# Kernel tuning notes

Hardware: AMD Instinct MI355X
Metric: run time of the kernel (lower is better)

Reference implementation:

```python
import jax, jax.numpy as jnp
import numpy as np


def rotary_pos_emb(x):
    # x: [b, h, l, k]; interleaved rotary embedding (pairs are (0,1),(2,3),...)
    dim = x.shape[-1]
    seq = x.shape[-2]
    ts = jnp.arange(0, dim, 2, dtype=jnp.float32)
    inv_freqs = 10000.0 ** (-ts / dim)                      # [dim/2]
    grid = jnp.arange(seq, dtype=jnp.float32)[:, None] * inv_freqs[None, :]  # [l, dim/2]
    sin_embs = jnp.repeat(jnp.sin(grid), 2, axis=-1)[None]  # [1, l, dim] (interleaved repeat)
    cos_embs = jnp.repeat(jnp.cos(grid), 2, axis=-1)[None]
    x1, x2 = x[..., ::2], x[..., 1::2]
    xs = jnp.stack([-x2, x1], axis=-1).reshape(x.shape)     # interleave (-x2, x1)
    return x * cos_embs + xs * sin_embs


def setup_inputs() -> dict:
    key = jax.random.key(0)
    ks = jax.random.split(key, 5)
    b, l, d = 2, 2048, 1024
    scale = 1.0 / np.sqrt(d)
    return {
        "x": jax.random.normal(ks[0], (b, l, d), dtype=jnp.float32),
        "Wq": jax.random.normal(ks[1], (d, d), dtype=jnp.float32) * scale,
        "Wk": jax.random.normal(ks[2], (d, d), dtype=jnp.float32) * scale,
        "Wv": jax.random.normal(ks[3], (d, d), dtype=jnp.float32) * scale,
        "Wo": jax.random.normal(ks[4], (d, d), dtype=jnp.float32) * scale,
        "is_training": 0,
    }


def reference(x, Wq, Wk, Wv, Wo, is_training):
    n_heads = 16
    b, l, d = x.shape
    k_size = d // n_heads
    # NOTE: module scales q by 1/sqrt(model_size), not 1/sqrt(key_size)
    q = (x @ Wq) / jnp.sqrt(jnp.float32(d))
    q = q.reshape(b, l, n_heads, k_size).transpose(0, 2, 1, 3)  # b h l k
    k = (x @ Wk).reshape(b, l, n_heads, k_size).transpose(0, 2, 1, 3)
    v = (x @ Wv).reshape(b, l, n_heads, k_size).transpose(0, 2, 1, 3)
    q = rotary_pos_emb(q)
    k = rotary_pos_emb(k)
    logits = jnp.einsum('bhik,bhjk->bhij', q, k)  # no mask, no dropout (eval)
    a = jax.nn.softmax(logits, axis=-1)
    y = jnp.einsum('bhij,bhjv->bhiv', a, v)
    y = y.transpose(0, 2, 1, 3).reshape(b, l, d)  # b l (h v)
    return y @ Wo
```

## Files before the change

kernel.cpp:

```cpp
#include <hip/hip_runtime.h>
#include <stdint.h>

typedef unsigned short u16;
typedef unsigned int u32;
using short8 = __attribute__((ext_vector_type(8))) short;
using f32x4  = __attribute__((ext_vector_type(4))) float;
using f32x16 = __attribute__((ext_vector_type(16))) float;

typedef __attribute__((address_space(1))) unsigned int gu32;
typedef __attribute__((address_space(3))) unsigned int lu32;

__device__ __forceinline__ void gl2lds16(const u16* g, u16* lds_wave_base) {
    __builtin_amdgcn_global_load_lds(
        (gu32*)(uintptr_t)(const void*)g,
        (lu32*)(uint32_t)(uintptr_t)(void*)lds_wave_base,
        16, 0, 0);
}

__device__ inline float bf2f(u16 u) {
    union { unsigned int i; float f; } v;
    v.i = ((unsigned int)u) << 16;
    return v.f;
}
__device__ inline u16 f2bf(float f) {
    union { float f; unsigned int i; } v;
    v.f = f;
    unsigned int x = v.i;
    return (u16)((x + 0x7fffu + ((x >> 16) & 1u)) >> 16);
}
__device__ inline u32 f2bf_trunc_u32(float f) {
    union { float f; unsigned int i; } v;
    v.f = f;
    return v.i >> 16;
}

__global__ __launch_bounds__(256) void prep(
    const float* __restrict__ x, u16* __restrict__ xb,
    const float* __restrict__ w0, const float* __restrict__ w1,
    const float* __restrict__ w2, const float* __restrict__ w3,
    u16* __restrict__ t0, u16* __restrict__ t1,
    u16* __restrict__ t2, u16* __restrict__ t3,
    float2* __restrict__ tab)
{
    int tx = threadIdx.x, ty = threadIdx.y;
    int tid = ty * 32 + tx;
    int z = blockIdx.z;
    if (z == 4) {
        int bidx = blockIdx.y * 32 + blockIdx.x;
        if (bidx < 256) {
            int idx = bidx * 256 + tid;
            int pos = idx >> 5, pi = idx & 31;
            const float l2_10000_over_32 = 0.41524101186f;
            float ang = (float)pos *
                __builtin_amdgcn_exp2f(-(float)pi * l2_10000_over_32);
            float sn, cs;
            __sincosf(ang, &sn, &cs);
            tab[idx] = make_float2(cs, sn);
        }
        return;
    }
    if (z >= 5) {
        int i = (((z - 5) * 1024 + blockIdx.y * 32 + blockIdx.x) * 256 + tid) * 4;
        float4 v = *(const float4*)(x + i);
        ushort4 o;
        o.x = f2bf(v.x); o.y = f2bf(v.y); o.z = f2bf(v.z); o.w = f2bf(v.w);
        *(ushort4*)(xb + i) = o;
        return;
    }
    __shared__ u16 tile[32][33];
    const float* src; u16* dst;
    switch (z) {
        case 0:  src = w0; dst = t0; break;
        case 1:  src = w1; dst = t1; break;
        case 2:  src = w2; dst = t2; break;
        default: src = w3; dst = t3; break;
    }
    int c0 = blockIdx.x * 32, r0 = blockIdx.y * 32;
    #pragma unroll
    for (int i = 0; i < 4; i++)
        tile[ty + i * 8][tx] = f2bf(src[(size_t)(r0 + ty + i * 8) * 1024 + c0 + tx]);
    __syncthreads();
    #pragma unroll
    for (int i = 0; i < 4; i++)
        dst[(size_t)(c0 + ty + i * 8) * 1024 + r0 + tx] = tile[tx][ty + i * 8];
}

__global__ __launch_bounds__(256) void gemm_qkv(
    const u16* __restrict__ A, const u16* __restrict__ Bt,
    const float2* __restrict__ ropetab,
    u16* __restrict__ Qb, u16* __restrict__ Kb, u16* __restrict__ VT)
{
    __shared__ __align__(16) char smem[128 * 136 * 2];
    u16* As = (u16*)smem;
    u16* Bs = (u16*)(smem + 16384);

    const int tid  = threadIdx.x;
    const int lane = tid & 63;
    const int wid  = tid >> 6;
    const int quad = lane >> 4;
    const int l15  = lane & 15;
    const int wm   = wid >> 1, wn = wid & 1;

    const int m0 = blockIdx.y * 128;
    const int n0 = blockIdx.x * 128;
    const int mat = n0 >> 10;
    const int ln0 = n0 & 1023;

    f32x4 acc[4][4] = {};

    for (int k0 = 0; k0 < 1024; k0 += 64) {
        #pragma unroll
        for (int it = 0; it < 4; it++) {
            int c   = it * 256 + tid;
            int row = c >> 3;
            int col = ((c & 7) ^ (row & 7)) * 8;
            u16* lbA = &As[(size_t)(it * 256 + wid * 64) * 8];
            u16* lbB = &Bs[(size_t)(it * 256 + wid * 64) * 8];
            gl2lds16(&A [(size_t)(m0 + row) * 1024 + k0 + col], lbA);
            gl2lds16(&Bt[(size_t)(n0 + row) * 1024 + k0 + col], lbB);
        }
        __syncthreads();

        #pragma unroll
        for (int s = 0; s < 2; s++) {
            short8 a[4], b[4];
            #pragma unroll
            for (int i = 0; i < 4; i++) {
                int ra = wm * 64 + i * 16 + l15;
                int rb = wn * 64 + i * 16 + l15;
                a[i] = *(const short8*)(&As[ra * 64 + (((s * 4 + quad) ^ (ra & 7)) * 8)]);
                b[i] = *(const short8*)(&Bs[rb * 64 + (((s * 4 + quad) ^ (rb & 7)) * 8)]);
            }
            #pragma unroll
            for (int i = 0; i < 4; i++)
                #pragma unroll
                for (int j = 0; j < 4; j++)
                    acc[i][j] = __builtin_amdgcn_mfma_f32_16x16x32_bf16(a[i], b[j], acc[i][j], 0, 0, 0);
        }
        __syncthreads();
    }

    if (mat < 2) {
        u16* C = (mat == 0) ? Qb : Kb;
        const float scale = (mat == 0) ? (0.03125f * 1.44269504f) : 1.0f;
        const int odd = l15 & 1;
        #pragma unroll
        for (int i = 0; i < 4; i++)
            #pragma unroll
            for (int j = 0; j < 4; j++)
                #pragma unroll
                for (int r = 0; r < 4; r++) {
                    int lrow = wm * 64 + i * 16 + quad * 4 + r;
                    int col  = ln0 + wn * 64 + j * 16 + l15;
                    int pos  = (m0 + lrow) & 2047;
                    float v  = acc[i][j][r] * scale;
                    float vp = __shfl_xor(v, 1);
                    float2 sc = ropetab[pos * 32 + ((col & 63) >> 1)];
                    float outv = odd ? (v * sc.x + vp * sc.y)
                                     : (v * sc.x - vp * sc.y);
                    C[(size_t)(m0 + lrow) * 1024 + col] = f2bf(outv);
                }
    } else {
        u16* T = (u16*)smem;
        __syncthreads();
        #pragma unroll
        for (int i = 0; i < 4; i++)
            #pragma unroll
            for (int j = 0; j < 4; j++)
                #pragma unroll
                for (int r = 0; r < 4; r++) {
                    int lrow = wm * 64 + i * 16 + quad * 4 + r;
                    int lcol = wn * 64 + j * 16 + l15;
                    T[lcol * 136 + lrow] = f2bf(acc[i][j][r]);
                }
        __syncthreads();
        int bb2 = m0 >> 11, pos0 = m0 & 2047;
        #pragma unroll
        for (int itc = 0; itc < 8; itc++) {
            int c  = itc * 256 + tid;
            int ch = c >> 4;
            int px = (c & 15) * 8;
            int head = (ln0 + ch) >> 6;
            size_t dst = ((size_t)(bb2 * 16 + head) * 64 + (ch & 63)) * 2048
                         + pos0 + px;
            *(uint4*)(&VT[dst]) = *(const uint4*)(&T[ch * 136 + px]);
        }
    }
}

__global__ __launch_bounds__(256) void gemm_out(
    const u16* __restrict__ A, const u16* __restrict__ Bt, float* __restrict__ C)
{
    __shared__ __align__(16) u16 As[128 * 64];
    __shared__ __align__(16) u16 Bs[128 * 64];

    const int tid  = threadIdx.x;
    const int lane = tid & 63;
    const int wid  = tid >> 6;
    const int quad = lane >> 4;
    const int l15  = lane & 15;
    const int wm   = wid >> 1, wn = wid & 1;

    const int m0 = blockIdx.y * 128;
    const int n0 = blockIdx.x * 128;

    f32x4 acc[4][4] = {};

    for (int k0 = 0; k0 < 1024; k0 += 64) {
        #pragma unroll
        for (int it = 0; it < 4; it++) {
            int c   = it * 256 + tid;
            int row = c >> 3;
            int col = ((c & 7) ^ (row & 7)) * 8;
            u16* lbA = &As[(size_t)(it * 256 + wid * 64) * 8];
            u16* lbB = &Bs[(size_t)(it * 256 + wid * 64) * 8];
            gl2lds16(&A [(size_t)(m0 + row) * 1024 + k0 + col], lbA);
            gl2lds16(&Bt[(size_t)(n0 + row) * 1024 + k0 + col], lbB);
        }
        __syncthreads();

        #pragma unroll
        for (int s = 0; s < 2; s++) {
            short8 a[4], b[4];
            #pragma unroll
            for (int i = 0; i < 4; i++) {
                int ra = wm * 64 + i * 16 + l15;
                int rb = wn * 64 + i * 16 + l15;
                a[i] = *(const short8*)(&As[ra * 64 + (((s * 4 + quad) ^ (ra & 7)) * 8)]);
                b[i] = *(const short8*)(&Bs[rb * 64 + (((s * 4 + quad) ^ (rb & 7)) * 8)]);
            }
            #pragma unroll
            for (int i = 0; i < 4; i++)
                #pragma unroll
                for (int j = 0; j < 4; j++)
                    acc[i][j] = __builtin_amdgcn_mfma_f32_16x16x32_bf16(a[i], b[j], acc[i][j], 0, 0, 0);
        }
        __syncthreads();
    }

    #pragma unroll
    for (int i = 0; i < 4; i++)
        #pragma unroll
        for (int j = 0; j < 4; j++)
            #pragma unroll
            for (int r = 0; r < 4; r++) {
                int row = m0 + wm * 64 + i * 16 + quad * 4 + r;
                int col = n0 + wn * 64 + j * 16 + l15;
                C[(size_t)row * 1024 + col] = acc[i][j][r];
            }
}

__global__ __launch_bounds__(256) void attn(
    const u16* __restrict__ Q, const u16* __restrict__ Kb,
    const u16* __restrict__ VT, u16* __restrict__ Y)
{
    __shared__ __align__(16) u16 Ks [128 * 64];
    __shared__ __align__(16) u16 VTs[64 * 128];
    __shared__ __align__(16) u16 Ps [4][32 * 72];

    const int tid  = threadIdx.x;
    const int lane = tid & 63, wid = tid >> 6;
    const int l31  = lane & 31, hi = lane >> 5;

    const int bh = blockIdx.x;
    const int qt = blockIdx.y;
    const int bb = bh >> 4, h = bh & 15;

    const size_t base = ((size_t)bb * 2048) * 1024 + (size_t)h * 64;

    short8 qf[4];
    {
        const u16* qp = Q + base
                      + ((size_t)qt * 128 + wid * 32 + l31) * 1024 + hi * 8;
        #pragma unroll
        for (int s = 0; s < 4; s++)
            qf[s] = *(const short8*)(qp + s * 16);
    }

    f32x16 o0 = {}, o1 = {};
    float lsum = 0.0f;

    for (int j0 = 0; j0 < 2048; j0 += 128) {
        __syncthreads();
        #pragma unroll
        for (int it = 0; it < 4; it++) {
            int c = it * 256 + tid;
            int rk = c >> 3, ck = ((c & 7)  ^ (rk & 7))  * 8;
            int rv = c >> 4, cv = ((c & 15) ^ (rv & 15)) * 8;
            u16* lbK = &Ks [(size_t)(it * 256 + wid * 64) * 8];
            u16* lbV = &VTs[(size_t)(it * 256 + wid * 64) * 8];
            gl2lds16(&Kb[base + (size_t)(j0 + rk) * 1024 + ck], lbK);
            gl2lds16(&VT[((size_t)bh * 64 + rv) * 2048 + j0 + cv], lbV);
        }
        __syncthreads();

        f32x16 st[4];
        #pragma unroll
        for (int t = 0; t < 4; t++) {
            int key = t * 32 + l31;
            f32x16 z = {};
            __builtin_amdgcn_s_setprio(1);
            #pragma unroll
            for (int s = 0; s < 4; s++) {
                int chunk = ((2 * s + hi) ^ (key & 7)) * 8;
                short8 kf = *(const short8*)(&Ks[key * 64 + chunk]);
                z = __builtin_amdgcn_mfma_f32_32x32x16_bf16(kf, qf[s], z, 0, 0, 0);
            }
            __builtin_amdgcn_s_setprio(0);
            st[t] = z;
        }

        u16* ps = Ps[wid];
        #pragma unroll
        for (int hh = 0; hh < 2; hh++) {
            #pragma unroll
            for (int tt = 0; tt < 2; tt++) {
                int t = hh * 2 + tt;
                #pragma unroll
                for (int g = 0; g < 4; g++) {
                    float p0 = __builtin_amdgcn_exp2f(st[t][4 * g + 0]);
                    float p1 = __builtin_amdgcn_exp2f(st[t][4 * g + 1]);
                    float p2 = __builtin_amdgcn_exp2f(st[t][4 * g + 2]);
                    float p3 = __builtin_amdgcn_exp2f(st[t][4 * g + 3]);
                    lsum += (p0 + p1) + (p2 + p3);
                    uint2 w;
                    w.x = f2bf_trunc_u32(p0) | (f2bf_trunc_u32(p1) << 16);
                    w.y = f2bf_trunc_u32(p2) | (f2bf_trunc_u32(p3) << 16);
                    int lk = tt * 32 + g * 8 + hi * 4;
                    *(uint2*)(&ps[l31 * 72 + lk]) = w;
                }
            }
            asm volatile("s_waitcnt lgkmcnt(0)" ::: "memory");

            #pragma unroll
            for (int s = 0; s < 4; s++) {
                int koff = s * 16 + hi * 8;
                short8 pf = *(const short8*)(&ps[l31 * 72 + koff]);
                int kch = hh * 8 + 2 * s + hi;
                short8 v0 = *(const short8*)(&VTs[l31 * 128 + ((kch ^ (l31 & 15)) * 8)]);
                short8 v1 = *(const short8*)(&VTs[(32 + l31) * 128 + ((kch ^ ((32 + l31) & 15)) * 8)]);
                __builtin_amdgcn_s_setprio(1);
                o0 = __builtin_amdgcn_mfma_f32_32x32x16_bf16(pf, v0, o0, 0, 0, 0);
                o1 = __builtin_amdgcn_mfma_f32_32x32x16_bf16(pf, v1, o1, 0, 0, 0);
                __builtin_amdgcn_s_setprio(0);
            }
            asm volatile("" ::: "memory");
        }
    }

    lsum += __shfl_xor(lsum, 32);
    float linv = 1.0f / lsum;

    size_t qrow0 = (size_t)qt * 128 + wid * 32;
    #pragma unroll
    for (int half = 0; half < 2; half++) {
        f32x16 o = half ? o1 : o0;
        #pragma unroll
        for (int reg = 0; reg < 16; reg++) {
            int qrow = (reg & 3) + 8 * (reg >> 2) + 4 * hi;
            float nv = o[reg] * __shfl(linv, qrow);
            Y[base + (qrow0 + qrow) * 1024 + half * 32 + l31] = f2bf(nv);
        }
    }
}

extern "C" void kernel_launch(void* const* d_in, const int* in_sizes, int n_in,
                              void* d_out, int out_size, void* d_ws, size_t ws_size,
                              hipStream_t stream)
{
    const float* x  = (const float*)d_in[0];
    const float* Wq = (const float*)d_in[1];
    const float* Wk = (const float*)d_in[2];
    const float* Wv = (const float*)d_in[3];
    const float* Wo = (const float*)d_in[4];
    float* out = (float*)d_out;

    char* ws = (char*)d_ws;
    u16*    xb    = (u16*)   (ws + (0ull  << 20));
    u16*    WqkvT = (u16*)   (ws + (8ull  << 20));
    u16*    WoT   = (u16*)   (ws + (14ull << 20));
    u16*    Qb    = (u16*)   (ws + (16ull << 20));
    u16*    Kb    = (u16*)   (ws + (24ull << 20));
    u16*    VTb   = (u16*)   (ws + (32ull << 20));
    u16*    Yb    = (u16*)   (ws + (40ull << 20));
    float2* tab   = (float2*)(ws + (48ull << 20));

    prep<<<dim3(32, 32, 9), dim3(32, 8), 0, stream>>>(
        x, xb, Wq, Wk, Wv, Wo,
        WqkvT, WqkvT + (1024ull * 1024), WqkvT + (2048ull * 1024), WoT, tab);
    gemm_qkv<<<dim3(24, 32), 256, 0, stream>>>(xb, WqkvT, tab, Qb, Kb, VTb);
    attn<<<dim3(32, 16), 256, 0, stream>>>(Qb, Kb, VTb, Yb);
    gemm_out<<<dim3(8, 32), 256, 0, stream>>>(Yb, WoT, out);
}
```

Baseline: 201.3 us.

## Prefetch next K/V tile into registers to overlap loads with attention compute

Replaces the direct global-to-LDS loads of each K and V^T tile with register staging. The next tile's global loads are issued into registers before the compute of the current tile, then written to LDS at the start of the next iteration. This is meant to hide global memory latency behind the QK^T/softmax/PV MFMA work. It adds eight uint4 registers per thread and sets a two-blocks-per-CU launch bound, which may constrain register allocation.

```diff
diff --git a/kernel.cpp b/kernel.cpp
--- a/kernel.cpp
+++ b/kernel.cpp
@@ -250,7 +250,7 @@
             }
 }
 
-__global__ __launch_bounds__(256) void attn(
+__global__ __launch_bounds__(256, 2) void attn(
     const u16* __restrict__ Q, const u16* __restrict__ Kb,
     const u16* __restrict__ VT, u16* __restrict__ Y)
 {
@@ -277,21 +277,54 @@
             qf[s] = *(const short8*)(qp + s * 16);
     }
 
+    const int c0 = tid,        c1 = 256 + tid,
+              c2 = 512 + tid,  c3 = 768 + tid;
+    const int rk0 = c0 >> 3, ck0 = ((c0 & 7) ^ (rk0 & 7)) * 8;
+    const int rk1 = c1 >> 3, ck1 = ((c1 & 7) ^ (rk1 & 7)) * 8;
+    const int rk2 = c2 >> 3, ck2 = ((c2 & 7) ^ (rk2 & 7)) * 8;
+    const int rk3 = c3 >> 3, ck3 = ((c3 & 7) ^ (rk3 & 7)) * 8;
+    const int rv0 = c0 >> 4, cv0 = ((c0 & 15) ^ (rv0 & 15)) * 8;
+    const int rv1 = c1 >> 4, cv1 = ((c1 & 15) ^ (rv1 & 15)) * 8;
+    const int rv2 = c2 >> 4, cv2 = ((c2 & 15) ^ (rv2 & 15)) * 8;
+    const int rv3 = c3 >> 4, cv3 = ((c3 & 15) ^ (rv3 & 15)) * 8;
+    const u16* pK = Kb + base;
+    const u16* pV = VT + ((size_t)bh * 64) * 2048;
+    const size_t oK0 = (size_t)rk0 * 1024 + ck0, oK1 = (size_t)rk1 * 1024 + ck1;
+    const size_t oK2 = (size_t)rk2 * 1024 + ck2, oK3 = (size_t)rk3 * 1024 + ck3;
+    const size_t oV0 = (size_t)rv0 * 2048 + cv0, oV1 = (size_t)rv1 * 2048 + cv1;
+    const size_t oV2 = (size_t)rv2 * 2048 + cv2, oV3 = (size_t)rv3 * 2048 + cv3;
+
+    uint4 k0r, k1r, k2r, k3r, v0r, v1r, v2r, v3r;
+#define LOADREGS(J0)                                                        \
+    do {                                                                    \
+        const size_t jk = (size_t)(J0) * 1024;                              \
+        k0r = *(const uint4*)(pK + jk + oK0);                               \
+        k1r = *(const uint4*)(pK + jk + oK1);                               \
+        k2r = *(const uint4*)(pK + jk + oK2);                               \
+        k3r = *(const uint4*)(pK + jk + oK3);                               \
+        v0r = *(const uint4*)(pV + (J0) + oV0);                             \
+        v1r = *(const uint4*)(pV + (J0) + oV1);                             \
+        v2r = *(const uint4*)(pV + (J0) + oV2);                             \
+        v3r = *(const uint4*)(pV + (J0) + oV3);                             \
+    } while (0)
+
     f32x16 o0 = {}, o1 = {};
     float lsum = 0.0f;
 
+    LOADREGS(0);
+
     for (int j0 = 0; j0 < 2048; j0 += 128) {
         __syncthreads();
-        #pragma unroll
-        for (int it = 0; it < 4; it++) {
-            int c = it * 256 + tid;
-            int rk = c >> 3, ck = ((c & 7)  ^ (rk & 7))  * 8;
-            int rv = c >> 4, cv = ((c & 15) ^ (rv & 15)) * 8;
-            u16* lbK = &Ks [(size_t)(it * 256 + wid * 64) * 8];
-            u16* lbV = &VTs[(size_t)(it * 256 + wid * 64) * 8];
-            gl2lds16(&Kb[base + (size_t)(j0 + rk) * 1024 + ck], lbK);
-            gl2lds16(&VT[((size_t)bh * 64 + rv) * 2048 + j0 + cv], lbV);
-        }
+        *(uint4*)(&Ks [(0 * 256 + tid) * 8]) = k0r;
+        *(uint4*)(&Ks [(1 * 256 + tid) * 8]) = k1r;
+        *(uint4*)(&Ks [(2 * 256 + tid) * 8]) = k2r;
+        *(uint4*)(&Ks [(3 * 256 + tid) * 8]) = k3r;
+        *(uint4*)(&VTs[(0 * 256 + tid) * 8]) = v0r;
+        *(uint4*)(&VTs[(1 * 256 + tid) * 8]) = v1r;
+        *(uint4*)(&VTs[(2 * 256 + tid) * 8]) = v2r;
+        *(uint4*)(&VTs[(3 * 256 + tid) * 8]) = v3r;
+        if (j0 + 128 < 2048)
+            LOADREGS(j0 + 128);
         __syncthreads();
 
         f32x16 st[4];
@@ -347,6 +380,7 @@
             asm volatile("" ::: "memory");
         }
     }
+#undef LOADREGS
 
     lsum += __shfl_xor(lsum, 32);
     float linv = 1.0f / lsum;
```

Result: no change. 198.0 us (-1.6%).
